# Optimization experiments

Hardware: AMD Instinct MI355X
Metric: run time of the kernel (lower is better)

Reference implementation:

```python
import jax, jax.numpy as jnp
import numpy as np

IGNORE_INDEX = -100
NEG_INF = -1e9
EPS_NORM = 1e-12
EPS_DENOM = 1e-8


def setup_inputs() -> dict:
    key = jax.random.key(0)
    k1, k2, k3 = jax.random.split(key, 3)
    B, T, V, D = 8, 512, 32128, 512
    logits = jax.random.normal(k1, (B, T, V), dtype=jnp.float32)
    labels = jax.random.randint(k2, (B, T), 0, V, dtype=jnp.int32)
    pad = jnp.arange(T)[None, :] >= (T - T // 8)
    labels = jnp.where(pad, IGNORE_INDEX, labels)
    embedding_matrix = jax.random.normal(k3, (V, D), dtype=jnp.float32) * 0.02
    return {"logits": logits, "labels": labels, "embedding_matrix": embedding_matrix}


def _l2norm(x):
    return x / jnp.maximum(jnp.linalg.norm(x, axis=-1, keepdims=True), EPS_NORM)


def reference(logits, labels, embedding_matrix):
    probs = jax.nn.softmax(logits.astype(jnp.float32), axis=-1)           # [B,T,V]
    soft_pred = jnp.einsum('btv,vd->btd', probs,
                           embedding_matrix.astype(jnp.float32))          # [B,T,D]
    safe_labels = jnp.where(labels == IGNORE_INDEX, 0, labels)
    hard_ref = embedding_matrix[safe_labels].astype(jnp.float32)          # [B,T,D]
    valid = (labels != IGNORE_INDEX)                                      # [B,T]

    p_n = _l2norm(soft_pred)
    r_n = _l2norm(hard_ref)
    sim = jnp.einsum('bid,bjd->bij', p_n, r_n)                            # [B,T,T]

    validf = valid.astype(jnp.float32)
    cnt = jnp.sum(validf, axis=1)                                         # [B]
    denom_cnt = jnp.maximum(cnt, 1.0)

    # precision: for each valid pred i, max sim over valid refs j
    sim_cols = jnp.where(valid[:, None, :], sim, NEG_INF)
    precision = jnp.sum(jnp.max(sim_cols, axis=2) * validf, axis=1) / denom_cnt
    # recall: for each valid ref j, max sim over valid preds i
    sim_rows = jnp.where(valid[:, :, None], sim, NEG_INF)
    recall = jnp.sum(jnp.max(sim_rows, axis=1) * validf, axis=1) / denom_cnt

    denom = precision + recall
    f1 = jnp.where(denom > 0,
                   2.0 * precision * recall / jnp.maximum(denom, EPS_DENOM),
                   jnp.zeros_like(denom))
    loss_b = jnp.where(cnt > 0, 1.0 - f1, 0.0)
    return jnp.mean(loss_b)
```

## Files before the change

### kernel.cpp

```cpp
#include <hip/hip_runtime.h>
#include <hip/hip_bf16.h>


#define IGNORE_INDEX (-100)
#define NEG_INF (-1e9f)

typedef float f32x4 __attribute__((ext_vector_type(4)));
typedef __bf16 bf16x8 __attribute__((ext_vector_type(8)));

static constexpr int BB = 8, T = 512, V = 32128, DD = 512;
static constexpr int R = BB * T;
static constexpr int KITERS = V / 32;
static constexpr int NCHUNK = 8;
static constexpr int CHUNK = (KITERS + NCHUNK - 1) / NCHUNK;

__device__ __forceinline__ unsigned short f2bf(float f) {
  unsigned u = __float_as_uint(f);
  u += 0x7fffu + ((u >> 16) & 1u);
  return (unsigned short)(u >> 16);
}
__device__ __forceinline__ unsigned pack2(float lo, float hi) {
  return (unsigned)f2bf(lo) | ((unsigned)f2bf(hi) << 16);
}
__device__ __forceinline__ unsigned fenc(float f) {
  unsigned u = __float_as_uint(f);
  return (u & 0x80000000u) ? ~u : (u | 0x80000000u);
}
__device__ __forceinline__ float fdec(unsigned e) {
  unsigned u = (e & 0x80000000u) ? (e & 0x7fffffffu) : ~e;
  return __uint_as_float(u);
}

__global__ void k0_init(float* __restrict__ soft, unsigned* __restrict__ rowmax,
                        unsigned* __restrict__ colmax) {
  int idx = blockIdx.x * 256 + threadIdx.x;
  if (idx < R * DD) soft[idx] = 0.0f;
  if (idx < R) { rowmax[idx] = fenc(NEG_INF); colmax[idx] = fenc(NEG_INF); }
}

__global__ void k1_transpose(const float* __restrict__ E, unsigned short* __restrict__ eT) {
  __shared__ unsigned short tile[64][72];
  const int vb = blockIdx.x * 64, db = blockIdx.y * 64;
  const int t = threadIdx.x;
  {
    const int vl = t >> 2, dq = t & 3;
    const float4* src = (const float4*)(E + (size_t)(vb + vl) * DD + db + dq * 16);
    float4 x0 = src[0], x1 = src[1], x2 = src[2], x3 = src[3];
    unsigned short* dst = &tile[vl][dq * 16];
    dst[0]=f2bf(x0.x); dst[1]=f2bf(x0.y); dst[2]=f2bf(x0.z); dst[3]=f2bf(x0.w);
    dst[4]=f2bf(x1.x); dst[5]=f2bf(x1.y); dst[6]=f2bf(x1.z); dst[7]=f2bf(x1.w);
    dst[8]=f2bf(x2.x); dst[9]=f2bf(x2.y); dst[10]=f2bf(x2.z); dst[11]=f2bf(x2.w);
    dst[12]=f2bf(x3.x); dst[13]=f2bf(x3.y); dst[14]=f2bf(x3.z); dst[15]=f2bf(x3.w);
  }
  __syncthreads();
  {
    const int dl = t >> 2, vq = t & 3;
    unsigned v[16];
#pragma unroll
    for (int j = 0; j < 16; ++j) v[j] = tile[vq * 16 + j][dl];
    uint4 w0, w1;
    w0.x = v[0] | (v[1] << 16);  w0.y = v[2] | (v[3] << 16);
    w0.z = v[4] | (v[5] << 16);  w0.w = v[6] | (v[7] << 16);
    w1.x = v[8] | (v[9] << 16);  w1.y = v[10] | (v[11] << 16);
    w1.z = v[12] | (v[13] << 16); w1.w = v[14] | (v[15] << 16);
    uint4* out = (uint4*)(eT + (size_t)(db + dl) * V + vb + vq * 16);
    out[0] = w0; out[1] = w1;
  }
}

__launch_bounds__(512, 2)
__global__ void k2_gemm(const float* __restrict__ logits,
                        const unsigned short* __restrict__ eT,
                        float* __restrict__ soft) {
  extern __shared__ unsigned short smem[];
  const int t = threadIdx.x;
  const int lane = t & 63, wid = t >> 6;
  const int wm = wid >> 2, wn = wid & 3;
  const int rowbase = blockIdx.x * 128;
  const int it0 = blockIdx.y * CHUNK;
  const int itEnd = (it0 + CHUNK < KITERS) ? (it0 + CHUNK) : KITERS;

  const int am = t >> 2, akq = t & 3;
  const int bn = t;

  f32x4 acc[4][8];
#pragma unroll
  for (int i = 0; i < 4; ++i)
#pragma unroll
    for (int j = 0; j < 8; ++j) { f32x4 z = {0.f, 0.f, 0.f, 0.f}; acc[i][j] = z; }

  {
    const float4* ag = (const float4*)(logits + (size_t)(rowbase + am) * V + it0 * 32 + akq * 8);
    float4 a0 = ag[0], a1 = ag[1];
    const uint4* bg = (const uint4*)(eT + (size_t)bn * V + it0 * 32);
    uint4 b0 = bg[0], b1 = bg[1], b2 = bg[2], b3 = bg[3];
    uint4 w;
    w.x = pack2(__expf(a0.x), __expf(a0.y));
    w.y = pack2(__expf(a0.z), __expf(a0.w));
    w.z = pack2(__expf(a1.x), __expf(a1.y));
    w.w = pack2(__expf(a1.z), __expf(a1.w));
    *(uint4*)(smem + am * 40 + akq * 8) = w;
    unsigned short* Bd = smem + 10240 + bn * 40;
    *(uint4*)(Bd + 0) = b0; *(uint4*)(Bd + 8) = b1;
    *(uint4*)(Bd + 16) = b2; *(uint4*)(Bd + 24) = b3;
  }
  __syncthreads();

  int cur = 0;
  for (int it = it0; it < itEnd; ++it) {
    const bool hasNext = (it + 1) < itEnd;
    float4 a0, a1; uint4 b0, b1, b2, b3;
    if (hasNext) {
      const float4* ag = (const float4*)(logits + (size_t)(rowbase + am) * V + (it + 1) * 32 + akq * 8);
      a0 = ag[0]; a1 = ag[1];
      const uint4* bg = (const uint4*)(eT + (size_t)bn * V + (it + 1) * 32);
      b0 = bg[0]; b1 = bg[1]; b2 = bg[2]; b3 = bg[3];
    }
    const unsigned short* As = smem + cur * 5120;
    const unsigned short* Bs = smem + 10240 + cur * 20480;
    bf16x8 af[4], bf[8];
#pragma unroll
    for (int fm = 0; fm < 4; ++fm) {
      int row = wm * 64 + fm * 16 + (lane & 15);
      af[fm] = *(const bf16x8*)(As + row * 40 + (lane >> 4) * 8);
    }
#pragma unroll
    for (int fn = 0; fn < 8; ++fn) {
      int col = wn * 128 + fn * 16 + (lane & 15);
      bf[fn] = *(const bf16x8*)(Bs + col * 40 + (lane >> 4) * 8);
    }
#pragma unroll
    for (int fm = 0; fm < 4; ++fm)
#pragma unroll
      for (int fn = 0; fn < 8; ++fn)
        acc[fm][fn] = __builtin_amdgcn_mfma_f32_16x16x32_bf16(af[fm], bf[fn], acc[fm][fn], 0, 0, 0);
    if (hasNext) {
      const int nb = cur ^ 1;
      uint4 w;
      w.x = pack2(__expf(a0.x), __expf(a0.y));
      w.y = pack2(__expf(a0.z), __expf(a0.w));
      w.z = pack2(__expf(a1.x), __expf(a1.y));
      w.w = pack2(__expf(a1.z), __expf(a1.w));
      *(uint4*)(smem + nb * 5120 + am * 40 + akq * 8) = w;
      unsigned short* Bd = smem + 10240 + nb * 20480 + bn * 40;
      *(uint4*)(Bd + 0) = b0; *(uint4*)(Bd + 8) = b1;
      *(uint4*)(Bd + 16) = b2; *(uint4*)(Bd + 24) = b3;
    }
    __syncthreads();
    cur ^= 1;
  }

#pragma unroll
  for (int fm = 0; fm < 4; ++fm)
#pragma unroll
    for (int fn = 0; fn < 8; ++fn)
#pragma unroll
      for (int r4 = 0; r4 < 4; ++r4) {
        int row = rowbase + wm * 64 + fm * 16 + ((lane >> 4) << 2) + r4;
        int col = wn * 128 + fn * 16 + (lane & 15);
        atomicAdd(&soft[(size_t)row * DD + col], acc[fm][fn][r4]);
      }
}

__global__ void k3_norm(const float* __restrict__ soft, const int* __restrict__ labels,
                        const float* __restrict__ E,
                        unsigned short* __restrict__ pnb, unsigned short* __restrict__ rnb) {
  const int r = blockIdx.x;
  const int t = threadIdx.x;
  const int lane = t & 63, wid = t >> 6;
  __shared__ float red[8];

  const float* row = soft + (size_t)r * DD;
  float v0 = row[t], v1 = row[t + 256];
  float ss = v0 * v0 + v1 * v1;
#pragma unroll
  for (int m = 1; m < 64; m <<= 1) ss += __shfl_xor(ss, m, 64);
  if (lane == 0) red[wid] = ss;
  __syncthreads();
  float s = red[0] + red[1] + red[2] + red[3];
  float sc = 1.0f / fmaxf(sqrtf(s), 1e-12f);
  pnb[(size_t)r * DD + t] = f2bf(v0 * sc);
  pnb[(size_t)r * DD + t + 256] = f2bf(v1 * sc);

  int lab = labels[r];
  int safe = (lab == IGNORE_INDEX) ? 0 : lab;
  const float* hrow = E + (size_t)safe * DD;
  float h0 = hrow[t], h1 = hrow[t + 256];
  float ss2 = h0 * h0 + h1 * h1;
#pragma unroll
  for (int m = 1; m < 64; m <<= 1) ss2 += __shfl_xor(ss2, m, 64);
  if (lane == 0) red[4 + wid] = ss2;
  __syncthreads();
  float s2 = red[4] + red[5] + red[6] + red[7];
  float sc2 = 1.0f / fmaxf(sqrtf(s2), 1e-12f);
  rnb[(size_t)r * DD + t] = f2bf(h0 * sc2);
  rnb[(size_t)r * DD + t + 256] = f2bf(h1 * sc2);
}

__global__ void k4_sim(const unsigned short* __restrict__ pnb,
                       const unsigned short* __restrict__ rnb,
                       const int* __restrict__ labels,
                       unsigned* __restrict__ rowmax, unsigned* __restrict__ colmax) {
  const int lane = threadIdx.x;
  const int jt = blockIdx.x, it = blockIdx.y, b = blockIdx.z;
  const int i0 = it * 64, j0 = jt * 64;
  const unsigned short* pb = pnb + (size_t)b * T * DD;
  const unsigned short* rb = rnb + (size_t)b * T * DD;

  f32x4 acc[4][4];
#pragma unroll
  for (int i = 0; i < 4; ++i)
#pragma unroll
    for (int j = 0; j < 4; ++j) { f32x4 z = {0.f, 0.f, 0.f, 0.f}; acc[i][j] = z; }

  for (int kt = 0; kt < 16; ++kt) {
    bf16x8 a[4], bb[4];
#pragma unroll
    for (int fm = 0; fm < 4; ++fm)
      a[fm] = *(const bf16x8*)(pb + (size_t)(i0 + fm * 16 + (lane & 15)) * DD + kt * 32 + (lane >> 4) * 8);
#pragma unroll
    for (int fn = 0; fn < 4; ++fn)
      bb[fn] = *(const bf16x8*)(rb + (size_t)(j0 + fn * 16 + (lane & 15)) * DD + kt * 32 + (lane >> 4) * 8);
#pragma unroll
    for (int fm = 0; fm < 4; ++fm)
#pragma unroll
      for (int fn = 0; fn < 4; ++fn)
        acc[fm][fn] = __builtin_amdgcn_mfma_f32_16x16x32_bf16(a[fm], bb[fn], acc[fm][fn], 0, 0, 0);
  }

  const int* labB = labels + b * T;
  bool vj[4];
#pragma unroll
  for (int fn = 0; fn < 4; ++fn) vj[fn] = labB[j0 + fn * 16 + (lane & 15)] != IGNORE_INDEX;
  bool vi[4][4];
#pragma unroll
  for (int fm = 0; fm < 4; ++fm)
#pragma unroll
    for (int r4 = 0; r4 < 4; ++r4)
      vi[fm][r4] = labB[i0 + fm * 16 + ((lane >> 4) << 2) + r4] != IGNORE_INDEX;

#pragma unroll
  for (int fm = 0; fm < 4; ++fm)
#pragma unroll
    for (int r4 = 0; r4 < 4; ++r4) {
      float v = NEG_INF;
#pragma unroll
      for (int fn = 0; fn < 4; ++fn)
        if (vj[fn]) v = fmaxf(v, acc[fm][fn][r4]);
      v = fmaxf(v, __shfl_xor(v, 1, 64));
      v = fmaxf(v, __shfl_xor(v, 2, 64));
      v = fmaxf(v, __shfl_xor(v, 4, 64));
      v = fmaxf(v, __shfl_xor(v, 8, 64));
      if ((lane & 15) == 0)
        atomicMax(&rowmax[b * T + i0 + fm * 16 + ((lane >> 4) << 2) + r4], fenc(v));
    }
#pragma unroll
  for (int fn = 0; fn < 4; ++fn) {
    float v = NEG_INF;
#pragma unroll
    for (int fm = 0; fm < 4; ++fm)
#pragma unroll
      for (int r4 = 0; r4 < 4; ++r4)
        if (vi[fm][r4]) v = fmaxf(v, acc[fm][fn][r4]);
    v = fmaxf(v, __shfl_xor(v, 16, 64));
    v = fmaxf(v, __shfl_xor(v, 32, 64));
    if (lane < 16)
      atomicMax(&colmax[b * T + j0 + fn * 16 + lane], fenc(v));
  }
}

__global__ void k5_final(const int* __restrict__ labels, const unsigned* __restrict__ rowmax,
                         const unsigned* __restrict__ colmax, float* __restrict__ out) {
  const int t = threadIdx.x;
  const int lane = t & 63, wid = t >> 6;
  __shared__ float redC[4], redP[4], redR[4];
  __shared__ float totalS;
  if (t == 0) totalS = 0.f;
  __syncthreads();
  for (int b = 0; b < BB; ++b) {
    float c = 0.f, sp = 0.f, sr = 0.f;
    for (int d = t; d < T; d += 256) {
      if (labels[b * T + d] != IGNORE_INDEX) {
        c += 1.f;
        sp += fdec(rowmax[b * T + d]);
        sr += fdec(colmax[b * T + d]);
      }
    }
#pragma unroll
    for (int m = 1; m < 64; m <<= 1) {
      c += __shfl_xor(c, m, 64);
      sp += __shfl_xor(sp, m, 64);
      sr += __shfl_xor(sr, m, 64);
    }
    if (lane == 0) { redC[wid] = c; redP[wid] = sp; redR[wid] = sr; }
    __syncthreads();
    if (t == 0) {
      float cnt = redC[0] + redC[1] + redC[2] + redC[3];
      float dc = fmaxf(cnt, 1.f);
      float P = (redP[0] + redP[1] + redP[2] + redP[3]) / dc;
      float Rc = (redR[0] + redR[1] + redR[2] + redR[3]) / dc;
      float den = P + Rc;
      float f1 = (den > 0.f) ? (2.f * P * Rc / fmaxf(den, 1e-8f)) : 0.f;
      totalS += (cnt > 0.f) ? (1.f - f1) : 0.f;
    }
    __syncthreads();
  }
  if (t == 0) out[0] = totalS / (float)BB;
}

extern "C" void kernel_launch(void* const* d_in, const int* in_sizes, int n_in,
                              void* d_out, int out_size, void* d_ws, size_t ws_size,
                              hipStream_t stream) {
  const float* logits = (const float*)d_in[0];
  const int* labels = (const int*)d_in[1];
  const float* E = (const float*)d_in[2];
  float* out = (float*)d_out;
  char* ws = (char*)d_ws;

  unsigned short* eT = (unsigned short*)(ws);
  float* soft        = (float*)(ws + 32899072);
  unsigned short* pnb = (unsigned short*)(ws + 41287680);
  unsigned short* rnb = (unsigned short*)(ws + 45481984);
  unsigned* rowmax   = (unsigned*)(ws + 49676288);
  unsigned* colmax   = (unsigned*)(ws + 49692672);

  hipFuncSetAttribute((const void*)k2_gemm, hipFuncAttributeMaxDynamicSharedMemorySize, 102400);

  k0_init<<<8192, 256, 0, stream>>>(soft, rowmax, colmax);
  k1_transpose<<<dim3(V / 64, DD / 64), 256, 0, stream>>>(E, eT);
  k2_gemm<<<dim3(R / 128, NCHUNK), 512, 102400, stream>>>(logits, eT, soft);
  k3_norm<<<R, 256, 0, stream>>>(soft, labels, E, pnb, rnb);
  k4_sim<<<dim3(8, 8, 8), 64, 0, stream>>>(pnb, rnb, labels, rowmax, colmax);
  k5_final<<<1, 256, 0, stream>>>(labels, rowmax, colmax, out);
}
```

Measured before the change: 953.2 us.

## Pre-pack embedding tiles and stream B via global_load_lds with XOR-swizzled LDS

The embedding-transpose kernel now writes E in per-K-iteration 32x512 tiles that already match the GEMM's shared-memory layout, with an XOR swizzle on the 16-byte chunks. The GEMM then copies B tiles straight from global memory into LDS with global_load_lds, skipping the register round-trip. A and B LDS tiles drop the padding in favour of the same swizzle, which shrinks dynamic shared memory from 100KB to 80KB. The aim is to cut VGPR pressure and LDS store instructions in the main loop and to avoid bank conflicts without padding, at the cost of relying on async direct-to-LDS loads being correctly ordered by the existing barrier.

```diff
diff --git a/kernel.cpp b/kernel.cpp
--- a/kernel.cpp
+++ b/kernel.cpp
@@ -30,6 +30,11 @@
   unsigned u = (e & 0x80000000u) ? (e & 0x7fffffffu) : ~e;
   return __uint_as_float(u);
 }
+__device__ __forceinline__ void gload16(const void* g, void* l) {
+  __builtin_amdgcn_global_load_lds(
+      (const __attribute__((address_space(1))) unsigned*)g,
+      (__attribute__((address_space(3))) unsigned*)l, 16, 0, 0);
+}
 
 __global__ void k0_init(float* __restrict__ soft, unsigned* __restrict__ rowmax,
                         unsigned* __restrict__ colmax) {
@@ -38,33 +43,50 @@
   if (idx < R) { rowmax[idx] = fenc(NEG_INF); colmax[idx] = fenc(NEG_INF); }
 }
 
-__global__ void k1_transpose(const float* __restrict__ E, unsigned short* __restrict__ eT) {
-  __shared__ unsigned short tile[64][72];
-  const int vb = blockIdx.x * 64, db = blockIdx.y * 64;
+__global__ void k1_pack(const float* __restrict__ E, unsigned short* __restrict__ eT) {
+  __shared__ unsigned short sm[32][520];
+  const int it = blockIdx.x;
+  const int v0 = it * 32;
   const int t = threadIdx.x;
   {
-    const int vl = t >> 2, dq = t & 3;
-    const float4* src = (const float4*)(E + (size_t)(vb + vl) * DD + db + dq * 16);
-    float4 x0 = src[0], x1 = src[1], x2 = src[2], x3 = src[3];
-    unsigned short* dst = &tile[vl][dq * 16];
-    dst[0]=f2bf(x0.x); dst[1]=f2bf(x0.y); dst[2]=f2bf(x0.z); dst[3]=f2bf(x0.w);
-    dst[4]=f2bf(x1.x); dst[5]=f2bf(x1.y); dst[6]=f2bf(x1.z); dst[7]=f2bf(x1.w);
-    dst[8]=f2bf(x2.x); dst[9]=f2bf(x2.y); dst[10]=f2bf(x2.z); dst[11]=f2bf(x2.w);
-    dst[12]=f2bf(x3.x); dst[13]=f2bf(x3.y); dst[14]=f2bf(x3.z); dst[15]=f2bf(x3.w);
+    const int row = t >> 3, colq = t & 7;
+    const float* src = E + (size_t)(v0 + row) * DD + colq * 4;
+#pragma unroll
+    for (int u = 0; u < 16; ++u) {
+      float4 x = *(const float4*)(src + u * 32);
+      uint2 w;
+      w.x = pack2(x.x, x.y);
+      w.y = pack2(x.z, x.w);
+      *(uint2*)&sm[row][colq * 4 + u * 32] = w;
+    }
   }
   __syncthreads();
   {
-    const int dl = t >> 2, vq = t & 3;
-    unsigned v[16];
-#pragma unroll
-    for (int j = 0; j < 16; ++j) v[j] = tile[vq * 16 + j][dl];
-    uint4 w0, w1;
-    w0.x = v[0] | (v[1] << 16);  w0.y = v[2] | (v[3] << 16);
-    w0.z = v[4] | (v[5] << 16);  w0.w = v[6] | (v[7] << 16);
-    w1.x = v[8] | (v[9] << 16);  w1.y = v[10] | (v[11] << 16);
-    w1.z = v[12] | (v[13] << 16); w1.w = v[14] | (v[15] << 16);
-    uint4* out = (uint4*)(eT + (size_t)(db + dl) * V + vb + vq * 16);
-    out[0] = w0; out[1] = w1;
+    const int c0 = 2 * t;
+    unsigned short va[32], vb[32];
+#pragma unroll
+    for (int v = 0; v < 32; ++v) {
+      unsigned w = *(const unsigned*)&sm[v][c0];
+      va[v] = (unsigned short)w;
+      vb[v] = (unsigned short)(w >> 16);
+    }
+    unsigned short* base = eT + (size_t)it * 16384;
+#pragma unroll
+    for (int cc = 0; cc < 2; ++cc) {
+      const int col = c0 + cc;
+      unsigned short* ob = base + col * 32;
+#pragma unroll
+      for (int k8 = 0; k8 < 4; ++k8) {
+        const unsigned short* vv = cc ? (vb + k8 * 8) : (va + k8 * 8);
+        uint4 w;
+        w.x = (unsigned)vv[0] | ((unsigned)vv[1] << 16);
+        w.y = (unsigned)vv[2] | ((unsigned)vv[3] << 16);
+        w.z = (unsigned)vv[4] | ((unsigned)vv[5] << 16);
+        w.w = (unsigned)vv[6] | ((unsigned)vv[7] << 16);
+        int k8p = k8 ^ ((col >> 1) & 3);
+        *(uint4*)(ob + k8p * 8) = w;
+      }
+    }
   }
 }
 
@@ -73,6 +95,8 @@
                         const unsigned short* __restrict__ eT,
                         float* __restrict__ soft) {
   extern __shared__ unsigned short smem[];
+  unsigned short* Asm = smem;
+  unsigned short* Bsm = smem + 8192;
   const int t = threadIdx.x;
   const int lane = t & 63, wid = t >> 6;
   const int wm = wid >> 2, wn = wid & 3;
@@ -81,7 +105,9 @@
   const int itEnd = (it0 + CHUNK < KITERS) ? (it0 + CHUNK) : KITERS;
 
   const int am = t >> 2, akq = t & 3;
-  const int bn = t;
+  const int aswz = akq ^ ((am >> 1) & 3);
+  const float* aG = logits + (size_t)(rowbase + am) * V + akq * 8;
+  const unsigned short* bG = eT + t * 8;
 
   f32x4 acc[4][8];
 #pragma unroll
@@ -90,61 +116,58 @@
     for (int j = 0; j < 8; ++j) { f32x4 z = {0.f, 0.f, 0.f, 0.f}; acc[i][j] = z; }
 
   {
-    const float4* ag = (const float4*)(logits + (size_t)(rowbase + am) * V + it0 * 32 + akq * 8);
-    float4 a0 = ag[0], a1 = ag[1];
-    const uint4* bg = (const uint4*)(eT + (size_t)bn * V + it0 * 32);
-    uint4 b0 = bg[0], b1 = bg[1], b2 = bg[2], b3 = bg[3];
+#pragma unroll
+    for (int i = 0; i < 4; ++i)
+      gload16(bG + (size_t)it0 * 16384 + i * 4096, Bsm + t * 8 + i * 4096);
+    float4 a0 = *(const float4*)(aG + (size_t)it0 * 32);
+    float4 a1 = *(const float4*)(aG + (size_t)it0 * 32 + 4);
     uint4 w;
     w.x = pack2(__expf(a0.x), __expf(a0.y));
     w.y = pack2(__expf(a0.z), __expf(a0.w));
     w.z = pack2(__expf(a1.x), __expf(a1.y));
     w.w = pack2(__expf(a1.z), __expf(a1.w));
-    *(uint4*)(smem + am * 40 + akq * 8) = w;
-    unsigned short* Bd = smem + 10240 + bn * 40;
-    *(uint4*)(Bd + 0) = b0; *(uint4*)(Bd + 8) = b1;
-    *(uint4*)(Bd + 16) = b2; *(uint4*)(Bd + 24) = b3;
+    *(uint4*)(Asm + am * 32 + aswz * 8) = w;
   }
   __syncthreads();
 
   int cur = 0;
   for (int it = it0; it < itEnd; ++it) {
+    const int nb = cur ^ 1;
     const bool hasNext = (it + 1) < itEnd;
-    float4 a0, a1; uint4 b0, b1, b2, b3;
+    float4 a0, a1;
     if (hasNext) {
-      const float4* ag = (const float4*)(logits + (size_t)(rowbase + am) * V + (it + 1) * 32 + akq * 8);
-      a0 = ag[0]; a1 = ag[1];
-      const uint4* bg = (const uint4*)(eT + (size_t)bn * V + (it + 1) * 32);
-      b0 = bg[0]; b1 = bg[1]; b2 = bg[2]; b3 = bg[3];
-    }
-    const unsigned short* As = smem + cur * 5120;
-    const unsigned short* Bs = smem + 10240 + cur * 20480;
-    bf16x8 af[4], bf[8];
+#pragma unroll
+      for (int i = 0; i < 4; ++i)
+        gload16(bG + (size_t)(it + 1) * 16384 + i * 4096,
+                Bsm + nb * 16384 + t * 8 + i * 4096);
+      a0 = *(const float4*)(aG + (size_t)(it + 1) * 32);
+      a1 = *(const float4*)(aG + (size_t)(it + 1) * 32 + 4);
+    }
+    const unsigned short* As = Asm + cur * 4096;
+    const unsigned short* Bs = Bsm + cur * 16384;
+    bf16x8 af[4], bfr[8];
 #pragma unroll
     for (int fm = 0; fm < 4; ++fm) {
       int row = wm * 64 + fm * 16 + (lane & 15);
-      af[fm] = *(const bf16x8*)(As + row * 40 + (lane >> 4) * 8);
+      af[fm] = *(const bf16x8*)(As + row * 32 + (((lane >> 4) ^ ((row >> 1) & 3)) << 3));
     }
 #pragma unroll
     for (int fn = 0; fn < 8; ++fn) {
       int col = wn * 128 + fn * 16 + (lane & 15);
-      bf[fn] = *(const bf16x8*)(Bs + col * 40 + (lane >> 4) * 8);
+      bfr[fn] = *(const bf16x8*)(Bs + col * 32 + (((lane >> 4) ^ ((col >> 1) & 3)) << 3));
     }
 #pragma unroll
     for (int fm = 0; fm < 4; ++fm)
 #pragma unroll
       for (int fn = 0; fn < 8; ++fn)
-        acc[fm][fn] = __builtin_amdgcn_mfma_f32_16x16x32_bf16(af[fm], bf[fn], acc[fm][fn], 0, 0, 0);
+        acc[fm][fn] = __builtin_amdgcn_mfma_f32_16x16x32_bf16(af[fm], bfr[fn], acc[fm][fn], 0, 0, 0);
     if (hasNext) {
-      const int nb = cur ^ 1;
       uint4 w;
       w.x = pack2(__expf(a0.x), __expf(a0.y));
       w.y = pack2(__expf(a0.z), __expf(a0.w));
       w.z = pack2(__expf(a1.x), __expf(a1.y));
       w.w = pack2(__expf(a1.z), __expf(a1.w));
-      *(uint4*)(smem + nb * 5120 + am * 40 + akq * 8) = w;
-      unsigned short* Bd = smem + 10240 + nb * 20480 + bn * 40;
-      *(uint4*)(Bd + 0) = b0; *(uint4*)(Bd + 8) = b1;
-      *(uint4*)(Bd + 16) = b2; *(uint4*)(Bd + 24) = b3;
+      *(uint4*)(Asm + nb * 4096 + am * 32 + aswz * 8) = w;
     }
     __syncthreads();
     cur ^= 1;
@@ -324,11 +347,11 @@
   unsigned* rowmax   = (unsigned*)(ws + 49676288);
   unsigned* colmax   = (unsigned*)(ws + 49692672);
 
-  hipFuncSetAttribute((const void*)k2_gemm, hipFuncAttributeMaxDynamicSharedMemorySize, 102400);
+  hipFuncSetAttribute((const void*)k2_gemm, hipFuncAttributeMaxDynamicSharedMemorySize, 81920);
 
   k0_init<<<8192, 256, 0, stream>>>(soft, rowmax, colmax);
-  k1_transpose<<<dim3(V / 64, DD / 64), 256, 0, stream>>>(E, eT);
-  k2_gemm<<<dim3(R / 128, NCHUNK), 512, 102400, stream>>>(logits, eT, soft);
+  k1_pack<<<KITERS, 256, 0, stream>>>(E, eT);
+  k2_gemm<<<dim3(R / 128, NCHUNK), 512, 81920, stream>>>(logits, eT, soft);
   k3_norm<<<R, 256, 0, stream>>>(soft, labels, E, pnb, rnb);
   k4_sim<<<dim3(8, 8, 8), 64, 0, stream>>>(pnb, rnb, labels, rowmax, colmax);
   k5_final<<<1, 256, 0, stream>>>(labels, rowmax, colmax, out);
```

Result: faster. 872.3 us (-8.5%).
